# Kernel optimization log

Measured on AMD Instinct MI355X. Metric: run time of the kernel, lower is better.

Reference implementation:

```python
import jax, jax.numpy as jnp
import numpy as np

N_NODES = 50000
N_EDGES = 1000000
IN_DIM = 256
N_ETYPE = 1000
L1_DIM = 16


def setup_inputs() -> dict:
    key = jax.random.key(0)
    ks = jax.random.split(key, 7)
    z = jax.random.normal(ks[0], (N_NODES, IN_DIM), dtype=jnp.float32)
    edge_index = jax.random.randint(ks[1], (2, N_EDGES), 0, N_NODES, dtype=jnp.int64)
    edge_type = jax.random.randint(ks[2], (N_EDGES,), 0, N_ETYPE, dtype=jnp.int64)
    w1_l1 = jax.random.normal(ks[3], (IN_DIM, L1_DIM), dtype=jnp.float32)
    w2_l1 = jax.random.normal(ks[4], (IN_DIM, L1_DIM), dtype=jnp.float32)
    std = 1.0 / np.sqrt(L1_DIM)
    w1_l2 = jax.random.normal(ks[5], (N_ETYPE, L1_DIM), dtype=jnp.float32) * std
    w2_l2 = jax.random.normal(ks[6], (N_ETYPE, L1_DIM), dtype=jnp.float32) * std
    return {"z": z, "edge_index": edge_index, "edge_type": edge_type,
            "w1_l1": w1_l1, "w1_l2": w1_l2, "w2_l1": w2_l1, "w2_l2": w2_l2}


def reference(z, edge_index, edge_type, w1_l1, w1_l2, w2_l1, w2_l2):
    # gather source/target node feats: [E, in_dim]
    d1 = jax.nn.relu(z[edge_index[0]] @ w1_l1)  # [E, l1_dim]
    d2 = jax.nn.relu(z[edge_index[1]] @ w2_l1)  # [E, l1_dim]
    s1 = jnp.sum(d1 * w1_l2[edge_type], axis=1)  # [E]
    s2 = jnp.sum(d2 * w2_l2[edge_type], axis=1)  # [E]
    return jax.nn.sigmoid(s1 + s2)
```

## Files before the change

kernel.cpp:

```cpp
#include <hip/hip_runtime.h>
#include <hip/hip_fp16.h>
#include <math.h>

#define IN_DIM 256
#define L1_DIM 16

typedef _Float16 f16x8 __attribute__((ext_vector_type(8)));
typedef float f32x4 __attribute__((ext_vector_type(4)));

__global__ __launch_bounds__(256) void proj_kernel(
    const float* __restrict__ z,
    const float* __restrict__ w1,
    const float* __restrict__ w2,
    const float* __restrict__ w1_l2,
    const float* __restrict__ w2_l2,
    __half* __restrict__ h1,
    __half* __restrict__ h2,
    __half* __restrict__ w1h,
    __half* __restrict__ w2h,
    int n_nodes, int nblocks_proj) {
  if ((int)blockIdx.x >= nblocks_proj) {
    int t0 = ((int)blockIdx.x - nblocks_proj) * 256 + (int)threadIdx.x;
    const int total = 1000 * L1_DIM;
    for (int i = t0; i < total; i += 8 * 256) {
      w1h[i] = __float2half(w1_l2[i]);
      w2h[i] = __float2half(w2_l2[i]);
    }
    return;
  }

  const int tid  = (int)threadIdx.x;
  const int lane = tid & 63;
  const int wv   = tid >> 6;
  const int r    = lane & 15;
  const int q    = lane >> 4;
  const int node0 = (int)blockIdx.x * 64;

  f16x8 bf1[8], bf2[8];
#pragma unroll
  for (int s = 0; s < 8; ++s) {
#pragma unroll
    for (int j = 0; j < 8; ++j) {
      int k = 32 * s + 8 * q + j;
      bf1[s][j] = (_Float16)w1[k * L1_DIM + r];
      bf2[s][j] = (_Float16)w2[k * L1_DIM + r];
    }
  }

  int arow = node0 + wv * 16 + r;
  int ar = arow < n_nodes ? arow : (n_nodes - 1);
  const float* zrow = z + (size_t)ar * IN_DIM + 8 * q;

  f32x4 acc1 = {0.f, 0.f, 0.f, 0.f};
  f32x4 acc2 = {0.f, 0.f, 0.f, 0.f};

#pragma unroll
  for (int s = 0; s < 8; ++s) {
    float4 lo = *reinterpret_cast<const float4*>(zrow + 32 * s);
    float4 hi = *reinterpret_cast<const float4*>(zrow + 32 * s + 4);
    f16x8 af;
    af[0] = (_Float16)lo.x; af[1] = (_Float16)lo.y;
    af[2] = (_Float16)lo.z; af[3] = (_Float16)lo.w;
    af[4] = (_Float16)hi.x; af[5] = (_Float16)hi.y;
    af[6] = (_Float16)hi.z; af[7] = (_Float16)hi.w;
    acc1 = __builtin_amdgcn_mfma_f32_16x16x32_f16(af, bf1[s], acc1, 0, 0, 0);
    acc2 = __builtin_amdgcn_mfma_f32_16x16x32_f16(af, bf2[s], acc2, 0, 0, 0);
  }

#pragma unroll
  for (int i = 0; i < 4; ++i) {
    int node = node0 + wv * 16 + 4 * q + i;
    if (node < n_nodes) {
      h1[(size_t)node * L1_DIM + r] = __float2half(fmaxf(acc1[i], 0.f));
      h2[(size_t)node * L1_DIM + r] = __float2half(fmaxf(acc2[i], 0.f));
    }
  }
}

__global__ __launch_bounds__(256) void edge_kernel(
    const int* __restrict__ edge_index,
    const int* __restrict__ edge_type,
    const __half* __restrict__ h1,
    const __half* __restrict__ h2,
    const __half* __restrict__ w1h,
    const __half* __restrict__ w2h,
    float* __restrict__ out,
    int n_edges) {
  int tid = (int)blockIdx.x * 256 + (int)threadIdx.x;
  int e = tid >> 1;
  int q = tid & 1;
  if (e >= n_edges) return;

  int src = edge_index[e];
  int dst = edge_index[n_edges + e];
  int t   = edge_type[e];

  float4 araw = *reinterpret_cast<const float4*>(h1  + (size_t)src * L1_DIM + q * 8);
  float4 braw = *reinterpret_cast<const float4*>(h2  + (size_t)dst * L1_DIM + q * 8);
  float4 uraw = *reinterpret_cast<const float4*>(w1h + (size_t)t   * L1_DIM + q * 8);
  float4 vraw = *reinterpret_cast<const float4*>(w2h + (size_t)t   * L1_DIM + q * 8);

  const __half2* A = reinterpret_cast<const __half2*>(&araw);
  const __half2* B = reinterpret_cast<const __half2*>(&braw);
  const __half2* U = reinterpret_cast<const __half2*>(&uraw);
  const __half2* V = reinterpret_cast<const __half2*>(&vraw);

  float s = 0.f;
#pragma unroll
  for (int p = 0; p < 4; ++p) {
    float2 af = __half22float2(A[p]);
    float2 uf = __half22float2(U[p]);
    float2 bf = __half22float2(B[p]);
    float2 vf = __half22float2(V[p]);
    s = fmaf(af.x, uf.x, s);
    s = fmaf(af.y, uf.y, s);
    s = fmaf(bf.x, vf.x, s);
    s = fmaf(bf.y, vf.y, s);
  }

  s += __shfl_xor(s, 1);

  if (q == 0) {
    out[e] = 1.0f / (1.0f + __expf(-s));
  }
}

extern "C" void kernel_launch(void* const* d_in, const int* in_sizes, int n_in,
                              void* d_out, int out_size, void* d_ws, size_t ws_size,
                              hipStream_t stream) {
  const float* z      = (const float*)d_in[0];
  const int* edge_idx = (const int*)d_in[1];
  const int* edge_typ = (const int*)d_in[2];
  const float* w1_l1  = (const float*)d_in[3];
  const float* w1_l2  = (const float*)d_in[4];
  const float* w2_l1  = (const float*)d_in[5];
  const float* w2_l2  = (const float*)d_in[6];
  float* out = (float*)d_out;

  int n_nodes = in_sizes[0] / IN_DIM;
  int n_edges = in_sizes[2];
  int n_l2    = in_sizes[4];

  __half* h1  = (__half*)d_ws;
  __half* h2  = h1 + (size_t)n_nodes * L1_DIM;
  __half* w1h = h2 + (size_t)n_nodes * L1_DIM;
  __half* w2h = w1h + (size_t)n_l2;

  {
    int nblocks_proj = (n_nodes + 63) / 64;
    int grid = nblocks_proj + 8;
    proj_kernel<<<grid, 256, 0, stream>>>(z, w1_l1, w2_l1, w1_l2, w2_l2,
                                          h1, h2, w1h, w2h,
                                          n_nodes, nblocks_proj);
  }
  {
    long long threads = (long long)n_edges * 2;
    int block = 256;
    int grid = (int)((threads + block - 1) / block);
    edge_kernel<<<grid, block, 0, stream>>>(edge_idx, edge_typ, h1, h2,
                                            w1h, w2h, out, n_edges);
  }
}
```

Before: 37.64 us.

## Stage interleaved edge-type weights in LDS with persistent edge kernel and fdot2

```diff
diff --git a/kernel.cpp b/kernel.cpp
--- a/kernel.cpp
+++ b/kernel.cpp
@@ -4,6 +4,7 @@
 
 #define IN_DIM 256
 #define L1_DIM 16
+#define N_ETYPE_MAX 1000
 
 typedef _Float16 f16x8 __attribute__((ext_vector_type(8)));
 typedef float f32x4 __attribute__((ext_vector_type(4)));
@@ -16,15 +17,15 @@
     const float* __restrict__ w2_l2,
     __half* __restrict__ h1,
     __half* __restrict__ h2,
-    __half* __restrict__ w1h,
-    __half* __restrict__ w2h,
-    int n_nodes, int nblocks_proj) {
+    __half* __restrict__ wq,
+    int n_nodes, int n_l2, int nblocks_proj) {
   if ((int)blockIdx.x >= nblocks_proj) {
     int t0 = ((int)blockIdx.x - nblocks_proj) * 256 + (int)threadIdx.x;
-    const int total = 1000 * L1_DIM;
-    for (int i = t0; i < total; i += 8 * 256) {
-      w1h[i] = __float2half(w1_l2[i]);
-      w2h[i] = __float2half(w2_l2[i]);
+    for (int i = t0; i < n_l2; i += 8 * 256) {
+      int t = i >> 4;
+      int j = i & 15;
+      wq[t * 32 + j]      = __float2half(w1_l2[i]);
+      wq[t * 32 + 16 + j] = __float2half(w2_l2[i]);
     }
     return;
   }
@@ -77,51 +78,64 @@
   }
 }
 
-__global__ __launch_bounds__(256) void edge_kernel(
+union F4H { float4 f; __half2 h[4]; };
+
+__global__ __launch_bounds__(512) void edge_kernel(
     const int* __restrict__ edge_index,
     const int* __restrict__ edge_type,
     const __half* __restrict__ h1,
     const __half* __restrict__ h2,
-    const __half* __restrict__ w1h,
-    const __half* __restrict__ w2h,
+    const __half* __restrict__ wq,
     float* __restrict__ out,
-    int n_edges) {
-  int tid = (int)blockIdx.x * 256 + (int)threadIdx.x;
-  int e = tid >> 1;
-  int q = tid & 1;
-  if (e >= n_edges) return;
+    int n_edges, int n_types) {
+  __shared__ __align__(16) __half wl[N_ETYPE_MAX * 32];
 
-  int src = edge_index[e];
-  int dst = edge_index[n_edges + e];
-  int t   = edge_type[e];
+  const int tid = (int)threadIdx.x;
 
-  float4 araw = *reinterpret_cast<const float4*>(h1  + (size_t)src * L1_DIM + q * 8);
-  float4 braw = *reinterpret_cast<const float4*>(h2  + (size_t)dst * L1_DIM + q * 8);
-  float4 uraw = *reinterpret_cast<const float4*>(w1h + (size_t)t   * L1_DIM + q * 8);
-  float4 vraw = *reinterpret_cast<const float4*>(w2h + (size_t)t   * L1_DIM + q * 8);
+  {
+    const float4* src = reinterpret_cast<const float4*>(wq);
+    float4* dst = reinterpret_cast<float4*>(wl);
+    int nf4 = n_types * 4;
+    for (int i = tid; i < nf4; i += 512) dst[i] = src[i];
+  }
+  __syncthreads();
 
-  const __half2* A = reinterpret_cast<const __half2*>(&araw);
-  const __half2* B = reinterpret_cast<const __half2*>(&braw);
-  const __half2* U = reinterpret_cast<const __half2*>(&uraw);
-  const __half2* V = reinterpret_cast<const __half2*>(&vraw);
+  const int q = tid & 1;
+  const int pair = tid >> 1;
+  const int stride = (int)gridDim.x * 256;
 
-  float s = 0.f;
+  for (int e = (int)blockIdx.x * 256 + pair; e < n_edges; e += stride) {
+    int src = edge_index[e];
+    int dst = edge_index[n_edges + e];
+    int t   = edge_type[e];
+
+    F4H a, b, u, v;
+    a.f = *reinterpret_cast<const float4*>(h1 + (size_t)src * L1_DIM + q * 8);
+    b.f = *reinterpret_cast<const float4*>(h2 + (size_t)dst * L1_DIM + q * 8);
+    u.f = *reinterpret_cast<const float4*>(wl + t * 32 + q * 8);
+    v.f = *reinterpret_cast<const float4*>(wl + t * 32 + 16 + q * 8);
+
+    float s = 0.f;
+#if __has_builtin(__builtin_amdgcn_fdot2)
 #pragma unroll
-  for (int p = 0; p < 4; ++p) {
-    float2 af = __half22float2(A[p]);
-    float2 uf = __half22float2(U[p]);
-    float2 bf = __half22float2(B[p]);
-    float2 vf = __half22float2(V[p]);
-    s = fmaf(af.x, uf.x, s);
-    s = fmaf(af.y, uf.y, s);
-    s = fmaf(bf.x, vf.x, s);
-    s = fmaf(bf.y, vf.y, s);
-  }
+    for (int p = 0; p < 4; ++p) {
+      s = __builtin_amdgcn_fdot2(a.h[p], u.h[p], s, false);
+      s = __builtin_amdgcn_fdot2(b.h[p], v.h[p], s, false);
+    }
+#else
+#pragma unroll
+    for (int p = 0; p < 4; ++p) {
+      float2 af = __half22float2(a.h[p]), uf = __half22float2(u.h[p]);
+      float2 bf = __half22float2(b.h[p]), vf = __half22float2(v.h[p]);
+      s = fmaf(af.x, uf.x, s); s = fmaf(af.y, uf.y, s);
+      s = fmaf(bf.x, vf.x, s); s = fmaf(bf.y, vf.y, s);
+    }
+#endif
 
-  s += __shfl_xor(s, 1);
-
-  if (q == 0) {
-    out[e] = 1.0f / (1.0f + __expf(-s));
+    s += __shfl_xor(s, 1);
+    if (q == 0) {
+      out[e] = 1.0f / (1.0f + __expf(-s));
+    }
   }
 }
 
@@ -140,24 +154,21 @@
   int n_nodes = in_sizes[0] / IN_DIM;
   int n_edges = in_sizes[2];
   int n_l2    = in_sizes[4];
+  int n_types = n_l2 / L1_DIM;
 
-  __half* h1  = (__half*)d_ws;
-  __half* h2  = h1 + (size_t)n_nodes * L1_DIM;
-  __half* w1h = h2 + (size_t)n_nodes * L1_DIM;
-  __half* w2h = w1h + (size_t)n_l2;
+  __half* h1 = (__half*)d_ws;
+  __half* h2 = h1 + (size_t)n_nodes * L1_DIM;
+  __half* wq = h2 + (size_t)n_nodes * L1_DIM;
 
   {
     int nblocks_proj = (n_nodes + 63) / 64;
     int grid = nblocks_proj + 8;
     proj_kernel<<<grid, 256, 0, stream>>>(z, w1_l1, w2_l1, w1_l2, w2_l2,
-                                          h1, h2, w1h, w2h,
-                                          n_nodes, nblocks_proj);
+                                          h1, h2, wq,
+                                          n_nodes, n_l2, nblocks_proj);
   }
   {
-    long long threads = (long long)n_edges * 2;
-    int block = 256;
-    int grid = (int)((threads + block - 1) / block);
-    edge_kernel<<<grid, block, 0, stream>>>(edge_idx, edge_typ, h1, h2,
-                                            w1h, w2h, out, n_edges);
+    edge_kernel<<<512, 512, 0, stream>>>(edge_idx, edge_typ, h1, h2, wq,
+                                         out, n_edges, n_types);
   }
 }
```

Result: faster. 34.51 us (-8.3%).
